# Performance work log

Measured on AMD Instinct MI355X. Metric: run time of the kernel, lower is better.

Reference implementation:

```python
import itertools
import jax, jax.numpy as jnp
import numpy as np

N_BLOCKS = 2_097_152  # number of 8x8 blocks; 512 MB fp32 input


def _make_alpha():
    a = np.array([1.0 / np.sqrt(2)] + [1.0] * 7)
    return jnp.asarray(np.outer(a, a), dtype=jnp.float32)  # [8,8]


def _make_dct_tensor():
    t = np.zeros((8, 8, 8, 8), dtype=np.float32)
    for x, y, u, v in itertools.product(range(8), repeat=4):
        t[x, y, u, v] = np.cos((2 * u + 1) * x * np.pi / 16) * np.cos((2 * v + 1) * y * np.pi / 16)
    return jnp.asarray(t)  # [8,8,8,8]


def setup_inputs() -> dict:
    key = jax.random.key(0)
    image = jax.random.normal(key, (N_BLOCKS, 8, 8), dtype=jnp.float32)
    return {"image": image, "alpha": _make_alpha(), "dct_tensor": _make_dct_tensor()}


def reference(image, alpha, dct_tensor):
    # result[n,u,v] = 0.25 * sum_{x,y} (image[n,x,y] * alpha[x,y]) * T[x,y,u,v] + 128
    scaled = image * alpha  # broadcast over batch of 8x8 blocks
    out = 0.25 * jnp.einsum("nxy,xyuv->nuv", scaled, dct_tensor) + 128.0
    return out
```

## Files before the change

kernel.cpp:

```cpp
#include <hip/hip_runtime.h>


#define WG      256
#define SETS    4
#define BLKWAVE 32
#define BLKWG   128
#define STRIDE4 17

template<bool FULL>
__device__ __forceinline__ void process_tile(
    const float4* __restrict__ in4, float4* __restrict__ o4,
    float4* __restrict__ lds4, const float* __restrict__ alpha,
    const float* __restrict__ dct, long long wgbase, int nblocks,
    int w, int b8, int r, int lane)
{
    const long long myblk0 = wgbase + w * BLKWAVE + b8;

    float4 lo[SETS], hi[SETS];
#pragma unroll
    for (int s = 0; s < SETS; ++s) {
        const long long g = myblk0 + s * 8;
        if (FULL || g < nblocks) {
            const size_t p = (size_t)g * 16 + r * 2;
            lo[s] = in4[p];
            hi[s] = in4[p + 1];
        } else {
            lo[s] = make_float4(0.f, 0.f, 0.f, 0.f);
            hi[s] = lo[s];
        }
    }

    float mv;
    {
        const int i = lane >> 3, j = lane & 7;
        mv = 0.5f * alpha[i * 8 + 1] * dct[i * 512 + j * 8];
    }
    float M[64];
#pragma unroll
    for (int k = 0; k < 64; ++k)
        M[k] = __int_as_float(__builtin_amdgcn_readlane(__float_as_int(mv), k));

    float mu[8];
#pragma unroll
    for (int x = 0; x < 8; ++x)
        mu[x] = 0.5f * alpha[x * 8 + 1] * dct[x * 512 + r * 8];

#pragma unroll
    for (int s = 0; s < SETS; ++s) {
        const float row[8] = {lo[s].x, lo[s].y, lo[s].z, lo[s].w,
                              hi[s].x, hi[s].y, hi[s].z, hi[s].w};
        float P[8];
#pragma unroll
        for (int v = 0; v < 8; ++v) {
            float acc = 0.0f;
#pragma unroll
            for (int y = 0; y < 8; ++y)
                acc = fmaf(row[y], M[y * 8 + v], acc);
            P[v] = acc;
        }
        float4* buf = &lds4[(w * BLKWAVE + s * 8 + b8) * STRIDE4];
        buf[r * 2 + 0] = make_float4(P[0], P[1], P[2], P[3]);
        buf[r * 2 + 1] = make_float4(P[4], P[5], P[6], P[7]);
    }

    asm volatile("s_waitcnt lgkmcnt(0)" ::: "memory");

#pragma unroll
    for (int s = 0; s < SETS; ++s) {
        const float4* buf = &lds4[(w * BLKWAVE + s * 8 + b8) * STRIDE4];
        float O[8] = {128.f, 128.f, 128.f, 128.f, 128.f, 128.f, 128.f, 128.f};
#pragma unroll
        for (int x = 0; x < 8; ++x) {
            const float4 plo = buf[x * 2 + 0];
            const float4 phi = buf[x * 2 + 1];
            const float m = mu[x];
            O[0] = fmaf(m, plo.x, O[0]);
            O[1] = fmaf(m, plo.y, O[1]);
            O[2] = fmaf(m, plo.z, O[2]);
            O[3] = fmaf(m, plo.w, O[3]);
            O[4] = fmaf(m, phi.x, O[4]);
            O[5] = fmaf(m, phi.y, O[5]);
            O[6] = fmaf(m, phi.z, O[6]);
            O[7] = fmaf(m, phi.w, O[7]);
        }
        const long long g = myblk0 + s * 8;
        if (FULL || g < nblocks) {
            const size_t p = (size_t)g * 16 + r * 2;
            o4[p]     = make_float4(O[0], O[1], O[2], O[3]);
            o4[p + 1] = make_float4(O[4], O[5], O[6], O[7]);
        }
    }
}

__global__ __launch_bounds__(WG, 4) void dct8x8_kernel(
    const float* __restrict__ image,
    const float* __restrict__ alpha,
    const float* __restrict__ dct,
    float* __restrict__ out,
    int nblocks)
{
    __shared__ float4 lds4[BLKWG * STRIDE4];

    const int t = threadIdx.x;
    const int w = t >> 6;
    const int lane = t & 63;
    const int b8 = lane >> 3;
    const int r = lane & 7;

    const long long wgbase = (long long)blockIdx.x * BLKWG;
    const float4* in4 = (const float4*)image;
    float4* o4 = (float4*)out;

    if (wgbase + BLKWG <= (long long)nblocks) {
        process_tile<true >(in4, o4, lds4, alpha, dct, wgbase, nblocks, w, b8, r, lane);
    } else {
        process_tile<false>(in4, o4, lds4, alpha, dct, wgbase, nblocks, w, b8, r, lane);
    }
}

extern "C" void kernel_launch(void* const* d_in, const int* in_sizes, int n_in,
                              void* d_out, int out_size, void* d_ws, size_t ws_size,
                              hipStream_t stream) {
    const float* image = (const float*)d_in[0];
    const float* alpha = (const float*)d_in[1];
    const float* dct   = (const float*)d_in[2];
    float* outp = (float*)d_out;

    const int nblocks = in_sizes[0] / 64;
    const long long wgs = ((long long)nblocks + BLKWG - 1) / BLKWG;

    dct8x8_kernel<<<(int)wgs, WG, 0, stream>>>(image, alpha, dct, outp, nblocks);
}
```

Measured before the change: 203.9 us.

## Use persistent grid-stride workgroups with register prefetch of next tile

Replaces the one-tile-per-workgroup launch with a persistent grid capped at 1024 workgroups. Each workgroup loops over tiles and issues the global loads for the next tile before computing and storing the current one. The aim is to overlap memory latency with compute and to amortise the per-workgroup setup (M readlane broadcast, mu loads) across many tiles. In exchange it uses more registers for the prefetched data, and a fixed grid of 1024 may not fully saturate HBM bandwidth on a memory-bound kernel.

```diff
diff --git a/kernel.cpp b/kernel.cpp
--- a/kernel.cpp
+++ b/kernel.cpp
@@ -3,30 +3,47 @@
 
 #define WG      256
 #define SETS    4
-#define BLKWAVE 32
 #define BLKWG   128
 #define STRIDE4 17
+#define NWG     1024
 
-template<bool FULL>
-__device__ __forceinline__ void process_tile(
-    const float4* __restrict__ in4, float4* __restrict__ o4,
-    float4* __restrict__ lds4, const float* __restrict__ alpha,
-    const float* __restrict__ dct, long long wgbase, int nblocks,
-    int w, int b8, int r, int lane)
+__global__ __launch_bounds__(WG, 4) void dct8x8_kernel(
+    const float* __restrict__ image,
+    const float* __restrict__ alpha,
+    const float* __restrict__ dct,
+    float* __restrict__ out,
+    int nblocks)
 {
-    const long long myblk0 = wgbase + w * BLKWAVE + b8;
+    __shared__ float4 lds4[BLKWG * STRIDE4];
 
-    float4 lo[SETS], hi[SETS];
+    const int t = threadIdx.x;
+    const int w = t >> 6;
+    const int lane = t & 63;
+    const int b8 = lane >> 3;
+    const int r = lane & 7;
+    const int myoff = w * 512 + b8 * 16 + r * 2;
+
+    const float4* __restrict__ in4 = (const float4*)image;
+    float4* __restrict__ o4 = (float4*)out;
+    const long long ntiles = ((long long)nblocks + BLKWG - 1) / BLKWG;
+
+    long long tile = blockIdx.x;
+    if (tile >= ntiles) return;
+
+    float4 c[2 * SETS];
+    {
+        const long long gb = tile * BLKWG;
+        const bool full = gb + BLKWG <= (long long)nblocks;
 #pragma unroll
-    for (int s = 0; s < SETS; ++s) {
-        const long long g = myblk0 + s * 8;
-        if (FULL || g < nblocks) {
-            const size_t p = (size_t)g * 16 + r * 2;
-            lo[s] = in4[p];
-            hi[s] = in4[p + 1];
-        } else {
-            lo[s] = make_float4(0.f, 0.f, 0.f, 0.f);
-            hi[s] = lo[s];
+        for (int s = 0; s < SETS; ++s) {
+            const long long g = gb + w * 32 + s * 8 + b8;
+            if (full || g < nblocks) {
+                const size_t p = (size_t)tile * 2048 + myoff + s * 128;
+                c[2 * s] = in4[p]; c[2 * s + 1] = in4[p + 1];
+            } else {
+                c[2 * s] = make_float4(0.f, 0.f, 0.f, 0.f);
+                c[2 * s + 1] = c[2 * s];
+            }
         }
     }
 
@@ -45,76 +62,82 @@
     for (int x = 0; x < 8; ++x)
         mu[x] = 0.5f * alpha[x * 8 + 1] * dct[x * 512 + r * 8];
 
+    while (true) {
+        const long long nxt = tile + gridDim.x;
+        const bool have = nxt < ntiles;
+        float4 n_[2 * SETS];
+        if (have) {
+            const long long gb = nxt * BLKWG;
+            const bool full = gb + BLKWG <= (long long)nblocks;
 #pragma unroll
-    for (int s = 0; s < SETS; ++s) {
-        const float row[8] = {lo[s].x, lo[s].y, lo[s].z, lo[s].w,
-                              hi[s].x, hi[s].y, hi[s].z, hi[s].w};
-        float P[8];
-#pragma unroll
-        for (int v = 0; v < 8; ++v) {
-            float acc = 0.0f;
-#pragma unroll
-            for (int y = 0; y < 8; ++y)
-                acc = fmaf(row[y], M[y * 8 + v], acc);
-            P[v] = acc;
+            for (int s = 0; s < SETS; ++s) {
+                const long long g = gb + w * 32 + s * 8 + b8;
+                if (full || g < nblocks) {
+                    const size_t p = (size_t)nxt * 2048 + myoff + s * 128;
+                    n_[2 * s] = in4[p]; n_[2 * s + 1] = in4[p + 1];
+                } else {
+                    n_[2 * s] = make_float4(0.f, 0.f, 0.f, 0.f);
+                    n_[2 * s + 1] = n_[2 * s];
+                }
+            }
         }
-        float4* buf = &lds4[(w * BLKWAVE + s * 8 + b8) * STRIDE4];
-        buf[r * 2 + 0] = make_float4(P[0], P[1], P[2], P[3]);
-        buf[r * 2 + 1] = make_float4(P[4], P[5], P[6], P[7]);
-    }
-
-    asm volatile("s_waitcnt lgkmcnt(0)" ::: "memory");
 
 #pragma unroll
-    for (int s = 0; s < SETS; ++s) {
-        const float4* buf = &lds4[(w * BLKWAVE + s * 8 + b8) * STRIDE4];
-        float O[8] = {128.f, 128.f, 128.f, 128.f, 128.f, 128.f, 128.f, 128.f};
+        for (int s = 0; s < SETS; ++s) {
+            const float row[8] = {c[2*s].x, c[2*s].y, c[2*s].z, c[2*s].w,
+                                  c[2*s+1].x, c[2*s+1].y, c[2*s+1].z, c[2*s+1].w};
+            float P[8];
 #pragma unroll
-        for (int x = 0; x < 8; ++x) {
-            const float4 plo = buf[x * 2 + 0];
-            const float4 phi = buf[x * 2 + 1];
-            const float m = mu[x];
-            O[0] = fmaf(m, plo.x, O[0]);
-            O[1] = fmaf(m, plo.y, O[1]);
-            O[2] = fmaf(m, plo.z, O[2]);
-            O[3] = fmaf(m, plo.w, O[3]);
-            O[4] = fmaf(m, phi.x, O[4]);
-            O[5] = fmaf(m, phi.y, O[5]);
-            O[6] = fmaf(m, phi.z, O[6]);
-            O[7] = fmaf(m, phi.w, O[7]);
+            for (int v = 0; v < 8; ++v) {
+                float acc = 0.0f;
+#pragma unroll
+                for (int y = 0; y < 8; ++y)
+                    acc = fmaf(row[y], M[y * 8 + v], acc);
+                P[v] = acc;
+            }
+            float4* buf = &lds4[(w * 32 + s * 8 + b8) * STRIDE4];
+            buf[r * 2 + 0] = make_float4(P[0], P[1], P[2], P[3]);
+            buf[r * 2 + 1] = make_float4(P[4], P[5], P[6], P[7]);
         }
-        const long long g = myblk0 + s * 8;
-        if (FULL || g < nblocks) {
-            const size_t p = (size_t)g * 16 + r * 2;
-            o4[p]     = make_float4(O[0], O[1], O[2], O[3]);
-            o4[p + 1] = make_float4(O[4], O[5], O[6], O[7]);
+
+        asm volatile("s_waitcnt lgkmcnt(0)" ::: "memory");
+
+        {
+            const long long gb = tile * BLKWG;
+            const bool full = gb + BLKWG <= (long long)nblocks;
+#pragma unroll
+            for (int s = 0; s < SETS; ++s) {
+                const float4* buf = &lds4[(w * 32 + s * 8 + b8) * STRIDE4];
+                float O[8] = {128.f,128.f,128.f,128.f,128.f,128.f,128.f,128.f};
+#pragma unroll
+                for (int x = 0; x < 8; ++x) {
+                    const float4 plo = buf[x * 2 + 0];
+                    const float4 phi = buf[x * 2 + 1];
+                    const float m = mu[x];
+                    O[0] = fmaf(m, plo.x, O[0]);
+                    O[1] = fmaf(m, plo.y, O[1]);
+                    O[2] = fmaf(m, plo.z, O[2]);
+                    O[3] = fmaf(m, plo.w, O[3]);
+                    O[4] = fmaf(m, phi.x, O[4]);
+                    O[5] = fmaf(m, phi.y, O[5]);
+                    O[6] = fmaf(m, phi.z, O[6]);
+                    O[7] = fmaf(m, phi.w, O[7]);
+                }
+                const long long g = gb + w * 32 + s * 8 + b8;
+                if (full || g < nblocks) {
+                    const size_t p = (size_t)tile * 2048 + myoff + s * 128;
+                    o4[p]     = make_float4(O[0], O[1], O[2], O[3]);
+                    o4[p + 1] = make_float4(O[4], O[5], O[6], O[7]);
+                }
+            }
         }
-    }
-}
 
-__global__ __launch_bounds__(WG, 4) void dct8x8_kernel(
-    const float* __restrict__ image,
-    const float* __restrict__ alpha,
-    const float* __restrict__ dct,
-    float* __restrict__ out,
-    int nblocks)
-{
-    __shared__ float4 lds4[BLKWG * STRIDE4];
+        asm volatile("" ::: "memory");
 
-    const int t = threadIdx.x;
-    const int w = t >> 6;
-    const int lane = t & 63;
-    const int b8 = lane >> 3;
-    const int r = lane & 7;
-
-    const long long wgbase = (long long)blockIdx.x * BLKWG;
-    const float4* in4 = (const float4*)image;
-    float4* o4 = (float4*)out;
-
-    if (wgbase + BLKWG <= (long long)nblocks) {
-        process_tile<true >(in4, o4, lds4, alpha, dct, wgbase, nblocks, w, b8, r, lane);
-    } else {
-        process_tile<false>(in4, o4, lds4, alpha, dct, wgbase, nblocks, w, b8, r, lane);
+        if (!have) break;
+#pragma unroll
+        for (int k = 0; k < 2 * SETS; ++k) c[k] = n_[k];
+        tile = nxt;
     }
 }
 
@@ -127,7 +150,9 @@
     float* outp = (float*)d_out;
 
     const int nblocks = in_sizes[0] / 64;
-    const long long wgs = ((long long)nblocks + BLKWG - 1) / BLKWG;
+    const long long ntiles = ((long long)nblocks + BLKWG - 1) / BLKWG;
+    int grid = (int)((ntiles < NWG) ? ntiles : NWG);
+    if (grid < 1) grid = 1;
 
-    dct8x8_kernel<<<(int)wgs, WG, 0, stream>>>(image, alpha, dct, outp, nblocks);
+    dct8x8_kernel<<<grid, WG, 0, stream>>>(image, alpha, dct, outp, nblocks);
 }
```

After: 214.3 us. 1.05x slower.
